# Kernel optimization log

Hardware: AMD Instinct MI355X
Metric: run time of the kernel (lower is better)

Reference implementation:

```python
import jax, jax.numpy as jnp
import numpy as np
import math


def _bandwidth(d):
    # gz = 2*Gamma((d+1)/2)/Gamma(d/2); use lgamma for numerical stability.
    gz = 2.0 * math.exp(math.lgamma(0.5 * (d + 1)) - math.lgamma(0.5 * d))
    return 1.0 / (2.0 * gz * gz)


def _kernel_mean(xa, xb, gamma):
    # mean over the [Na, Nb] RBF kernel matrix, squared distance via matmul identity
    sq = (jnp.sum(xa * xa, axis=1)[:, None]
          + jnp.sum(xb * xb, axis=1)[None, :]
          - 2.0 * (xa @ xb.T))
    sq = jnp.maximum(sq, 0.0)  # guard tiny negatives from the identity
    return jnp.mean(jnp.exp(-gamma * sq))


def setup_inputs() -> dict:
    key = jax.random.key(0)
    k1, k2 = jax.random.split(key)
    x1 = jax.random.normal(k1, (8192, 128), dtype=jnp.float32)
    x2 = jax.random.normal(k2, (8192, 128), dtype=jnp.float32)
    return {"x1": x1, "x2": x2}


def reference(x1, x2):
    g1 = _bandwidth(x1.shape[1])
    g2 = _bandwidth(x2.shape[1])
    m11 = _kernel_mean(x1, x1, g1)
    m22 = _kernel_mean(x2, x2, g2)
    m12 = _kernel_mean(x1, x2, g1)
    return jnp.sqrt(m11 - 2.0 * m12 + m22)
```

## Files before the change

kernel.cpp:

```cpp
#include <hip/hip_runtime.h>
#include <cmath>

#define D 128
#define BM 128
#define NSEG 8
#define LOG2E 1.4426950408889634

typedef __attribute__((ext_vector_type(8))) _Float16 f16x8;
typedef __attribute__((ext_vector_type(4))) float f32x4;
typedef __attribute__((ext_vector_type(2))) float f32x2;

__device__ __forceinline__ void async_cp16(const void* g, void* l) {
    __builtin_amdgcn_global_load_lds(
        (__attribute__((address_space(1))) void*)g,
        (__attribute__((address_space(3))) void*)l, 16, 0, 0);
}

__global__ __launch_bounds__(256) void prep_kernel(
    const float* __restrict__ x1, const float* __restrict__ x2,
    _Float16* __restrict__ xh, float* __restrict__ El,
    double* __restrict__ acc, float gl, int N) {
    int tid = threadIdx.x;
    if (blockIdx.x == 0 && tid < 64) acc[tid] = 0.0;
    int r = blockIdx.x * 16 + (tid >> 4);
    if (r >= 2 * N) return;
    int l = tid & 15;
    const float* row = (r < N) ? x1 + (size_t)r * D : x2 + (size_t)(r - N) * D;
    float4 v0 = ((const float4*)row)[l * 2];
    float4 v1 = ((const float4*)row)[l * 2 + 1];
    float v[8] = {v0.x, v0.y, v0.z, v0.w, v1.x, v1.y, v1.z, v1.w};
    float p = 0.f;
    _Float16 h8[8];
#pragma unroll
    for (int j = 0; j < 8; ++j) {
        p = fmaf(v[j], v[j], p);
        h8[j] = (_Float16)v[j];
    }
    *(uint4*)(xh + (size_t)r * D + l * 8) = *(uint4*)h8;
#pragma unroll
    for (int off = 8; off; off >>= 1) p += __shfl_down(p, off, 16);
    if (l == 0) El[r] = gl * p;
}

__global__ __launch_bounds__(512, 4) void mmd_mfma_kernel(
    const _Float16* __restrict__ xh, const float* __restrict__ El,
    double* __restrict__ acc, float c2l, int N) {
    __shared__ float4 smem[2][2048];

    int tid = threadIdx.x;
    int lane = tid & 63, wave = tid >> 6;
    int quad = lane >> 4, l16 = lane & 15;
    int wrow = (wave & 1) * 64;
    int wcol = (wave >> 1) * 32;

    int nt2 = 2 * N / BM;
    int half = N / BM;
    int p = blockIdx.x >> 3;
    int s = blockIdx.x & (NSEG - 1);
    int tpp = nt2 + 1;
    int q = tpp / NSEG, r = tpp % NSEG;
    int t0 = s * q + (s < r ? s : r);
    int nt = q + (s < r ? 1 : 0);

    int goff[4];
#pragma unroll
    for (int i = 0; i < 4; ++i) {
        int slot = i * 512 + tid;
        int row = slot >> 4;
        int g = (slot & 15) ^ (row & 7);
        goff[i] = row * D + g * 8;
    }

    auto stage = [&](int bBase, int buf) {
        const _Float16* src = xh + (size_t)bBase * D;
#pragma unroll
        for (int i = 0; i < 4; ++i)
            async_cp16(src + goff[i], &smem[buf][i * 512 + tid]);
    };
    auto BI = [&](int tt) { return tt <= p ? p : nt2 - 1 - p; };
    auto BJ = [&](int tt) { return tt <= p ? tt : tt - p - 1; };

    stage(BJ(t0) * BM, 0);
    stage(BJ(t0 + 1) * BM, 1);

    f16x8 a[4][4];
    int curA = -1;
    double dsum = 0.0;

    for (int i = 0; i < nt; ++i) {
        int tt = t0 + i;
        int bi = BI(tt), bj = BJ(tt);
        int aBase = bi * BM, bBase = bj * BM;
        float w = (bi == bj) ? 1.0f : 2.0f;
        if ((bi < half) != (bj < half)) w = -2.0f;
        int cur = i & 1;

        if (i + 1 < nt) {
            asm volatile("s_waitcnt vmcnt(4)" ::: "memory");
        } else {
            asm volatile("s_waitcnt vmcnt(0)" ::: "memory");
        }
        __builtin_amdgcn_s_barrier();
        __builtin_amdgcn_sched_barrier(0);

        if (aBase != curA) {
            curA = aBase;
#pragma unroll
            for (int u = 0; u < 4; ++u) {
                int ar = aBase + wrow + u * 16 + l16;
#pragma unroll
                for (int j = 0; j < 4; ++j) {
                    int g = (j >> 1) * 8 + (j & 1) * 4 + quad;
                    a[u][j] = *(const f16x8*)(xh + (size_t)ar * D + g * 8);
                }
            }
        }

        f32x4 C[4][2];
#pragma unroll
        for (int ti = 0; ti < 4; ++ti)
#pragma unroll
            for (int tj = 0; tj < 2; ++tj) C[ti][tj] = {0.f, 0.f, 0.f, 0.f};

        __builtin_amdgcn_s_setprio(1);
#pragma unroll
        for (int j = 0; j < 4; ++j) {
            int gb = (j >> 1) * 8 + (j & 1) * 4 + quad;
            f16x8 b[2];
#pragma unroll
            for (int u = 0; u < 2; ++u) {
                int br = wcol + u * 16 + l16;
                b[u] = *(const f16x8*)&smem[cur][br * 16 + (gb ^ (br & 7))];
            }
#pragma unroll
            for (int ti = 0; ti < 4; ++ti)
#pragma unroll
                for (int tj = 0; tj < 2; ++tj)
                    C[ti][tj] = __builtin_amdgcn_mfma_f32_16x16x32_f16(
                        a[ti][j], b[tj], C[ti][tj], 0, 0, 0);
        }
        __builtin_amdgcn_s_setprio(0);

        int arow0 = aBase + wrow + quad * 4;
        float4 ea4[4];
#pragma unroll
        for (int ti = 0; ti < 4; ++ti)
            ea4[ti] = *(const float4*)&El[arow0 + ti * 16];
        int bcol0 = bBase + wcol + l16;
        float ebv[2];
#pragma unroll
        for (int tj = 0; tj < 2; ++tj) ebv[tj] = El[bcol0 + tj * 16];

        f32x2 cc = {c2l, c2l};
        float lsum = 0.f;
#pragma unroll
        for (int tj = 0; tj < 2; ++tj) {
            f32x2 p2 = {0.f, 0.f};
#pragma unroll
            for (int ti = 0; ti < 4; ++ti) {
                f32x4 d = C[ti][tj];
                f32x2 a01 = cc * f32x2{d.x, d.y} + f32x2{ea4[ti].x, ea4[ti].y};
                f32x2 a23 = cc * f32x2{d.z, d.w} + f32x2{ea4[ti].z, ea4[ti].w};
                f32x2 e, e2;
                e.x = __builtin_amdgcn_exp2f(a01.x);
                e.y = __builtin_amdgcn_exp2f(a01.y);
                e2.x = __builtin_amdgcn_exp2f(a23.x);
                e2.y = __builtin_amdgcn_exp2f(a23.y);
                p2 += e + e2;
            }
            lsum = fmaf(p2.x + p2.y, __builtin_amdgcn_exp2f(ebv[tj]), lsum);
        }
        dsum += (double)lsum * (double)w;

        __builtin_amdgcn_sched_barrier(0);
        __builtin_amdgcn_s_barrier();
        __builtin_amdgcn_sched_barrier(0);
        if (i + 2 < nt) stage(BJ(tt + 2) * BM, cur);
    }

#pragma unroll
    for (int off = 32; off; off >>= 1) dsum += __shfl_down(dsum, off);
    double* red = (double*)&smem[0][0];
    if (lane == 0) red[wave] = dsum;
    __syncthreads();
    if (tid == 0) {
        double t8 = 0.0;
#pragma unroll
        for (int wv = 0; wv < 8; ++wv) t8 += red[wv];
        atomicAdd(&acc[blockIdx.x & 63], t8);
    }
}

__global__ __launch_bounds__(64) void mmd_finalize_kernel(
    const double* __restrict__ acc, float* __restrict__ out, int N) {
    int l = threadIdx.x;
    double v = acc[l];
#pragma unroll
    for (int off = 32; off; off >>= 1) v += __shfl_down(v, off);
    if (l == 0) {
        double nn = (double)N * (double)N;
        double s = v / nn;
        out[0] = (float)sqrt(s > 0.0 ? s : 0.0);
    }
}

extern "C" void kernel_launch(void* const* d_in, const int* in_sizes, int n_in,
                              void* d_out, int out_size, void* d_ws, size_t ws_size,
                              hipStream_t stream) {
    const float* x1 = (const float*)d_in[0];
    const float* x2 = (const float*)d_in[1];
    int N = in_sizes[0] / D;

    double* acc = (double*)d_ws;
    float* El = (float*)((char*)d_ws + 8192);
    _Float16* xh = (_Float16*)((char*)d_ws + 73728);

    double lg = lgamma(0.5 * (D + 1)) - lgamma(0.5 * D);
    double gz = 2.0 * exp(lg);
    double gamma = 1.0 / (2.0 * gz * gz);
    float gl = (float)(-gamma * LOG2E);
    float c2l = (float)(2.0 * gamma * LOG2E);

    prep_kernel<<<(2 * N + 15) / 16, 256, 0, stream>>>(x1, x2, xh, El, acc, gl, N);

    int nt2 = 2 * N / BM;
    int nblocks = (nt2 / 2) * NSEG;
    mmd_mfma_kernel<<<nblocks, 512, 0, stream>>>(xh, El, acc, c2l, N);

    mmd_finalize_kernel<<<1, 64, 0, stream>>>(acc, (float*)d_out, N);
}
```

Measured before the change: 118.2 us.

## Split MMD tiles into 128x64 halves with 256-thread blocks and more segments

Blocks shrink from 8 waves to 4 waves, and each 128x128 tile is processed as two 128x64 column halves. The A fragments and their row norms are loaded once per tile and reused across both halves. The number of segments per diagonal pair rises from 8 to 12, giving 768 blocks instead of 512, which is meant to spread work more evenly across CUs and improve latency hiding. The LDS footprint per block halves. The block count is now hardcoded as 64*NSEG, which only matches N=8192.

```diff
diff --git a/kernel.cpp b/kernel.cpp
--- a/kernel.cpp
+++ b/kernel.cpp
@@ -3,7 +3,8 @@
 
 #define D 128
 #define BM 128
-#define NSEG 8
+#define BN 64
+#define NSEG 12
 #define LOG2E 1.4426950408889634
 
 typedef __attribute__((ext_vector_type(8))) _Float16 f16x8;
@@ -42,10 +43,10 @@
     if (l == 0) El[r] = gl * p;
 }
 
-__global__ __launch_bounds__(512, 4) void mmd_mfma_kernel(
+__global__ __launch_bounds__(256, 3) void mmd_mfma_kernel(
     const _Float16* __restrict__ xh, const float* __restrict__ El,
     double* __restrict__ acc, float c2l, int N) {
-    __shared__ float4 smem[2][2048];
+    __shared__ float4 smem[2][1024];
 
     int tid = threadIdx.x;
     int lane = tid & 63, wave = tid >> 6;
@@ -55,53 +56,60 @@
 
     int nt2 = 2 * N / BM;
     int half = N / BM;
-    int p = blockIdx.x >> 3;
-    int s = blockIdx.x & (NSEG - 1);
+    int p = blockIdx.x / NSEG;
+    int s = blockIdx.x % NSEG;
     int tpp = nt2 + 1;
     int q = tpp / NSEG, r = tpp % NSEG;
     int t0 = s * q + (s < r ? s : r);
     int nt = q + (s < r ? 1 : 0);
+    int H = 2 * nt;
 
     int goff[4];
 #pragma unroll
     for (int i = 0; i < 4; ++i) {
-        int slot = i * 512 + tid;
+        int slot = i * 256 + tid;
         int row = slot >> 4;
         int g = (slot & 15) ^ (row & 7);
         goff[i] = row * D + g * 8;
     }
 
-    auto stage = [&](int bBase, int buf) {
-        const _Float16* src = xh + (size_t)bBase * D;
+    auto stage = [&](int b2Base, int buf) {
+        const _Float16* src = xh + (size_t)b2Base * D;
 #pragma unroll
         for (int i = 0; i < 4; ++i)
-            async_cp16(src + goff[i], &smem[buf][i * 512 + tid]);
+            async_cp16(src + goff[i], &smem[buf][i * 256 + tid]);
     };
     auto BI = [&](int tt) { return tt <= p ? p : nt2 - 1 - p; };
     auto BJ = [&](int tt) { return tt <= p ? tt : tt - p - 1; };
 
     stage(BJ(t0) * BM, 0);
-    stage(BJ(t0 + 1) * BM, 1);
+    stage(BJ(t0) * BM + BN, 1);
 
     f16x8 a[4][4];
+    float4 ea4[4];
     int curA = -1;
     double dsum = 0.0;
 
-    for (int i = 0; i < nt; ++i) {
-        int tt = t0 + i;
+    for (int ht = 0; ht < H; ++ht) {
+        int tt = t0 + (ht >> 1), h = ht & 1;
         int bi = BI(tt), bj = BJ(tt);
-        int aBase = bi * BM, bBase = bj * BM;
+        int aBase = bi * BM;
+        int bcolBase = bj * BM + h * BN;
         float w = (bi == bj) ? 1.0f : 2.0f;
         if ((bi < half) != (bj < half)) w = -2.0f;
-        int cur = i & 1;
-
-        if (i + 1 < nt) {
+        int cur = ht & 1;
+
+        if (ht + 1 < H) {
             asm volatile("s_waitcnt vmcnt(4)" ::: "memory");
         } else {
             asm volatile("s_waitcnt vmcnt(0)" ::: "memory");
         }
         __builtin_amdgcn_s_barrier();
         __builtin_amdgcn_sched_barrier(0);
+
+        int bcol0 = bcolBase + wcol + l16;
+        float ebv0 = El[bcol0];
+        float ebv1 = El[bcol0 + 16];
 
         if (aBase != curA) {
             curA = aBase;
@@ -114,7 +122,12 @@
                     a[u][j] = *(const f16x8*)(xh + (size_t)ar * D + g * 8);
                 }
             }
-        }
+            int arow0 = aBase + wrow + quad * 4;
+#pragma unroll
+            for (int ti = 0; ti < 4; ++ti)
+                ea4[ti] = *(const float4*)&El[arow0 + ti * 16];
+        }
+        __builtin_amdgcn_sched_barrier(0);
 
         f32x4 C[4][2];
 #pragma unroll
@@ -140,16 +153,6 @@
                         a[ti][j], b[tj], C[ti][tj], 0, 0, 0);
         }
         __builtin_amdgcn_s_setprio(0);
-
-        int arow0 = aBase + wrow + quad * 4;
-        float4 ea4[4];
-#pragma unroll
-        for (int ti = 0; ti < 4; ++ti)
-            ea4[ti] = *(const float4*)&El[arow0 + ti * 16];
-        int bcol0 = bBase + wcol + l16;
-        float ebv[2];
-#pragma unroll
-        for (int tj = 0; tj < 2; ++tj) ebv[tj] = El[bcol0 + tj * 16];
 
         f32x2 cc = {c2l, c2l};
         float lsum = 0.f;
@@ -168,14 +171,18 @@
                 e2.y = __builtin_amdgcn_exp2f(a23.y);
                 p2 += e + e2;
             }
-            lsum = fmaf(p2.x + p2.y, __builtin_amdgcn_exp2f(ebv[tj]), lsum);
+            lsum = fmaf(p2.x + p2.y,
+                        __builtin_amdgcn_exp2f(tj ? ebv1 : ebv0), lsum);
         }
         dsum += (double)lsum * (double)w;
 
         __builtin_amdgcn_sched_barrier(0);
         __builtin_amdgcn_s_barrier();
         __builtin_amdgcn_sched_barrier(0);
-        if (i + 2 < nt) stage(BJ(tt + 2) * BM, cur);
+        if (ht + 2 < H) {
+            int tn = t0 + ((ht + 2) >> 1);
+            stage(BJ(tn) * BM + h * BN, cur);
+        }
     }
 
 #pragma unroll
@@ -183,12 +190,8 @@
     double* red = (double*)&smem[0][0];
     if (lane == 0) red[wave] = dsum;
     __syncthreads();
-    if (tid == 0) {
-        double t8 = 0.0;
-#pragma unroll
-        for (int wv = 0; wv < 8; ++wv) t8 += red[wv];
-        atomicAdd(&acc[blockIdx.x & 63], t8);
-    }
+    if (tid == 0)
+        atomicAdd(&acc[blockIdx.x & 63], red[0] + red[1] + red[2] + red[3]);
 }
 
 __global__ __launch_bounds__(64) void mmd_finalize_kernel(
@@ -223,9 +226,8 @@
 
     prep_kernel<<<(2 * N + 15) / 16, 256, 0, stream>>>(x1, x2, xh, El, acc, gl, N);
 
-    int nt2 = 2 * N / BM;
-    int nblocks = (nt2 / 2) * NSEG;
-    mmd_mfma_kernel<<<nblocks, 512, 0, stream>>>(xh, El, acc, c2l, N);
+    int nblocks = 64 * NSEG;
+    mmd_mfma_kernel<<<nblocks, 256, 0, stream>>>(xh, El, acc, c2l, N);
 
     mmd_finalize_kernel<<<1, 64, 0, stream>>>(acc, (float*)d_out, N);
 }
```

After: 105.9 us, median of 2. -10.4%, faster.
